# Optimization experiments

Measured on AMD Instinct MI355X. Metric: run time of the kernel, lower is better.

The kernel has to match this reference:

```python
import jax, jax.numpy as jnp
import numpy as np

B, LQ, C = 4, 4096, 384
NH, NL, NP = 6, 1, 4
HL, WL = 64, 64
LV = HL * WL
DH = C // NH
EPS = 1e-6


def layer_norm(x, g, b):
    mu = jnp.mean(x, axis=-1, keepdims=True)
    var = jnp.mean(jnp.square(x - mu), axis=-1, keepdims=True)
    return (x - mu) * jax.lax.rsqrt(var + EPS) * g + b


def ms_deform_attn_core(value, spatial_shapes, level_start_index, loc, attn_w):
    # value [B,LV,NH,DH]; loc [B,LQ,NH,NL,NP,2] in [0,1]; attn_w [B,LQ,NH,NL,NP]
    ss = np.asarray(spatial_shapes)
    lsi = np.asarray(level_start_index)
    Bv, _, nH, dh = value.shape
    Lq = loc.shape[1]
    nP = loc.shape[4]
    out = jnp.zeros((Bv, Lq, nH, dh), value.dtype)
    for l in range(loc.shape[3]):
        Hl, Wl = int(ss[l, 0]), int(ss[l, 1])
        st = int(lsi[l])
        vflat = value[:, st:st + Hl * Wl]  # [B, Hl*Wl, nH, dh]
        xy = loc[:, :, :, l]               # [B,LQ,nH,NP,2]
        # grid_sample(align_corners=False): pixel = loc * size - 0.5
        x = xy[..., 0] * Wl - 0.5
        y = xy[..., 1] * Hl - 0.5
        x0 = jnp.floor(x)
        y0 = jnp.floor(y)
        wx = x - x0
        wy = y - y0
        x0i = x0.astype(jnp.int32)
        y0i = y0.astype(jnp.int32)

        def gather(xi, yi):
            # zero padding outside the feature map (padding_mode='zeros')
            valid = (xi >= 0) & (xi < Wl) & (yi >= 0) & (yi < Hl)
            idx = jnp.clip(yi, 0, Hl - 1) * Wl + jnp.clip(xi, 0, Wl - 1)  # [B,LQ,nH,NP]
            idx2 = idx.transpose(0, 1, 3, 2).reshape(Bv, Lq * nP, nH)
            g = jnp.take_along_axis(vflat, idx2[..., None], axis=1)       # [B,LQ*NP,nH,dh]
            g = g.reshape(Bv, Lq, nP, nH, dh).transpose(0, 1, 3, 2, 4)    # [B,LQ,nH,NP,dh]
            return g * valid[..., None].astype(value.dtype)

        samp = (gather(x0i, y0i) * ((1 - wx) * (1 - wy))[..., None]
                + gather(x0i + 1, y0i) * (wx * (1 - wy))[..., None]
                + gather(x0i, y0i + 1) * ((1 - wx) * wy)[..., None]
                + gather(x0i + 1, y0i + 1) * (wx * wy)[..., None])
        out = out + jnp.einsum('bqhpd,bqhp->bqhd', samp, attn_w[:, :, :, l])
    return out.reshape(Bv, Lq, nH * dh)


def setup_inputs() -> dict:
    key = jax.random.key(0)
    ks = jax.random.split(key, 12)
    s = 0.02
    return {
        'query': jax.random.normal(ks[0], (B, LQ, C), jnp.float32),
        'reference_points': jax.random.uniform(ks[1], (B, LQ, NL, 2), dtype=jnp.float32),
        'feat': jax.random.normal(ks[2], (B, LV, C), jnp.float32),
        'spatial_shapes': jnp.array([[HL, WL]], jnp.int32),
        'level_start_index': jnp.array([0], jnp.int32),
        'ln_q_g': jnp.ones((C,), jnp.float32), 'ln_q_b': jnp.zeros((C,), jnp.float32),
        'ln_f_g': jnp.ones((C,), jnp.float32), 'ln_f_b': jnp.zeros((C,), jnp.float32),
        'gamma': jax.random.normal(ks[3], (C,), jnp.float32) * 0.1,
        'Wv': jax.random.normal(ks[4], (C, C), jnp.float32) * s,
        'bv': jnp.zeros((C,), jnp.float32),
        'Wo': jax.random.normal(ks[5], (C, NH * NL * NP * 2), jnp.float32) * s,
        'bo': jax.random.normal(ks[6], (NH * NL * NP * 2,), jnp.float32) * 0.5,
        'Wa': jax.random.normal(ks[7], (C, NH * NL * NP), jnp.float32) * s,
        'ba': jnp.zeros((NH * NL * NP,), jnp.float32),
        'Wout': jax.random.normal(ks[8], (C, C), jnp.float32) * s,
        'bout': jnp.zeros((C,), jnp.float32),
    }


def reference(query, reference_points, feat, spatial_shapes, level_start_index,
              ln_q_g, ln_q_b, ln_f_g, ln_f_b, gamma,
              Wv, bv, Wo, bo, Wa, ba, Wout, bout):
    q = layer_norm(query, ln_q_g, ln_q_b)
    f = layer_norm(feat, ln_f_g, ln_f_b)
    value = (f @ Wv + bv).reshape(B, LV, NH, DH)
    offsets = (q @ Wo + bo).reshape(B, LQ, NH, NL, NP, 2)
    attn_w = jax.nn.softmax((q @ Wa + ba).reshape(B, LQ, NH, NL * NP), axis=-1)
    attn_w = attn_w.reshape(B, LQ, NH, NL, NP)
    # offset normalizer is (W, H) per level
    norm = jnp.stack([spatial_shapes[:, 1], spatial_shapes[:, 0]], -1).astype(jnp.float32)
    loc = reference_points[:, :, None, :, None, :] + offsets / norm[None, None, None, :, None, :]
    attn = ms_deform_attn_core(value, spatial_shapes, level_start_index, loc, attn_w)
    attn = attn @ Wout + bout
    return query + gamma * attn
```

## Files before the change

### kernel.cpp

```cpp
#include <hip/hip_runtime.h>
#include <math.h>

#define B_    4
#define LQ_   4096
#define C_    384
#define NH_   6
#define NP_   4
#define HL_   64
#define WL_   64
#define LV_   (HL_ * WL_)
#define ROWS_ (B_ * LQ_)
#define EPS_  1e-6f
#define NOFF_ 48
#define NLOG_ 24
#define WCTR_ 96

typedef unsigned short u16;
typedef unsigned int   u32;
typedef __bf16 bf16x8 __attribute__((ext_vector_type(8)));
typedef float  f32x4  __attribute__((ext_vector_type(4)));

__device__ __forceinline__ u16 f2bf(float f) {
    u32 u = __float_as_uint(f);
    u += 0x7fff + ((u >> 16) & 1);
    return (u16)(u >> 16);
}
__device__ __forceinline__ u32 pack2bf(float a, float b) {
    return (u32)f2bf(a) | ((u32)f2bf(b) << 16);
}

__device__ __forceinline__ f32x4 mfma16(bf16x8 a, bf16x8 b, f32x4 c) {
    return __builtin_amdgcn_mfma_f32_16x16x32_bf16(a, b, c, 0, 0, 0);
}

__device__ __forceinline__ void gl_lds16(const u16* g, u16* l) {
    __builtin_amdgcn_global_load_lds(
        (const __attribute__((address_space(1))) unsigned int*)g,
        (__attribute__((address_space(3))) unsigned int*)l, 16, 0, 0);
}

__device__ __forceinline__ void vm_wait8() { asm volatile("s_waitcnt vmcnt(8)" ::: "memory"); }
__device__ __forceinline__ void vm_wait7() { asm volatile("s_waitcnt vmcnt(7)" ::: "memory"); }
__device__ __forceinline__ void vm_wait0() { asm volatile("s_waitcnt vmcnt(0)" ::: "memory"); }
__device__ __forceinline__ void lgkm0()    { asm volatile("s_waitcnt lgkmcnt(0)" ::: "memory"); }
__device__ __forceinline__ void barrier_() { asm volatile("s_barrier" ::: "memory"); }

#define LN_BLOCKS_   8192
#define PREP_BLOCKS_ 1297

__global__ __launch_bounds__(256) void ln_prep(
    const float* __restrict__ query, const float* __restrict__ feat,
    const float* __restrict__ qg, const float* __restrict__ qbv,
    const float* __restrict__ fg, const float* __restrict__ fbv,
    u16* __restrict__ qout, u16* __restrict__ fout,
    const float* __restrict__ Wv, const float* __restrict__ Wout,
    const float* __restrict__ Wo, const float* __restrict__ Wa,
    const float* __restrict__ bo, const float* __restrict__ ba,
    u16* __restrict__ WvT, u16* __restrict__ WoutT, u16* __restrict__ WcT,
    float* __restrict__ bias_c)
{
    if (blockIdx.x < LN_BLOCKS_) {
        int wid  = threadIdx.x >> 6;
        int lane = threadIdx.x & 63;
        int row  = blockIdx.x * 4 + wid;
        const float *src, *g, *bsh;
        u16* dst;
        int r;
        if (row < ROWS_) { src = query; g = qg; bsh = qbv; dst = qout; r = row; }
        else             { src = feat;  g = fg; bsh = fbv; dst = fout; r = row - ROWS_; }

        const float* x = src + (size_t)r * C_;
        float4 a4 = *(const float4*)(x + 4 * lane);
        float2 a2 = *(const float2*)(x + 256 + 2 * lane);
        float v0 = a4.x, v1 = a4.y, v2 = a4.z, v3 = a4.w, v4 = a2.x, v5 = a2.y;

        float s = v0 + v1 + v2 + v3 + v4 + v5;
#pragma unroll
        for (int off = 32; off; off >>= 1) s += __shfl_xor(s, off);
        float mu = s * (1.f / C_);

        float d0 = v0 - mu, d1 = v1 - mu, d2 = v2 - mu;
        float d3 = v3 - mu, d4 = v4 - mu, d5 = v5 - mu;
        float s2 = d0*d0 + d1*d1 + d2*d2 + d3*d3 + d4*d4 + d5*d5;
#pragma unroll
        for (int off = 32; off; off >>= 1) s2 += __shfl_xor(s2, off);
        float rs = rsqrtf(s2 * (1.f / C_) + EPS_);

        float4 g4 = *(const float4*)(g + 4 * lane);
        float4 b4 = *(const float4*)(bsh + 4 * lane);
        float2 g2 = *(const float2*)(g + 256 + 2 * lane);
        float2 b2 = *(const float2*)(bsh + 256 + 2 * lane);

        float o0 = d0 * rs * g4.x + b4.x;
        float o1 = d1 * rs * g4.y + b4.y;
        float o2 = d2 * rs * g4.z + b4.z;
        float o3 = d3 * rs * g4.w + b4.w;
        float o4 = d4 * rs * g2.x + b2.x;
        float o5 = d5 * rs * g2.y + b2.y;

        u16* y = dst + (size_t)r * C_;
        uint2 w0; w0.x = pack2bf(o0, o1); w0.y = pack2bf(o2, o3);
        *(uint2*)(y + 4 * lane) = w0;
        *(u32*)(y + 256 + 2 * lane) = pack2bf(o4, o5);
    } else {
        const int KN = 384 * 384;
        int idx = (blockIdx.x - LN_BLOCKS_) * 256 + threadIdx.x;
        if (idx < KN) {
            int n = idx / 384, k = idx - n * 384;
            WvT[idx] = f2bf(Wv[k * 384 + n]);
        } else if (idx < 2 * KN) {
            int t = idx - KN;
            int n = t / 384, k = t - n * 384;
            WoutT[t] = f2bf(Wout[k * 384 + n]);
        } else if (idx < 2 * KN + WCTR_ * 384) {
            int t = idx - 2 * KN;
            int n = t / 384, k = t - n * 384;
            float v = (n < 48) ? Wo[k * 48 + n] : (n < 72 ? Wa[k * 24 + (n - 48)] : 0.f);
            WcT[t] = f2bf(v);
        } else if (idx < 2 * KN + WCTR_ * 384 + 80) {
            int n = idx - (2 * KN + WCTR_ * 384);
            bias_c[n] = (n < 48) ? bo[n] : (n < 72 ? ba[n - 48] : 0.f);
        }
    }
}

__global__ __launch_bounds__(256) void gemm_combined(
    const u16* __restrict__ fb, const u16* __restrict__ qb,
    const u16* __restrict__ WvT, const u16* __restrict__ WcT,
    const float* __restrict__ bv, const float* __restrict__ bias_c,
    u16* __restrict__ valb, float* __restrict__ offs, float* __restrict__ logits)
{
    __shared__ __align__(16) u16 As_[2][8192];
    __shared__ __align__(16) u16 Bs_[2][8192];

    int g    = blockIdx.x;
    int tid  = threadIdx.x;
    int lane = tid & 63, wid = tid >> 6;
    int fr = lane & 15, quad = lane >> 4;

    int swz  = (fr & 7) * 8;
    int off0 = (quad * 8) ^ swz;

    int srow = tid >> 3;
    int csw  = ((tid & 7) ^ (srow & 7)) * 8;

    if (g < 384) {
        int m0 = (g & 127) * 128, n0 = (g >> 7) * 128;
        const u16* aSrc = fb  + (size_t)(m0 + srow) * 384 + csw;
        const u16* bSrc = WvT + (size_t)(n0 + srow) * 384 + csw;

        int wm = (wid >> 1) * 64, wn = (wid & 1) * 64;

        f32x4 zero = {0.f, 0.f, 0.f, 0.f};
        f32x4 acc[4][4];
#pragma unroll
        for (int i = 0; i < 4; ++i)
#pragma unroll
            for (int j = 0; j < 4; ++j) acc[i][j] = zero;

#define STGV(bu, t) { _Pragma("unroll") for (int l = 0; l < 4; ++l) { \
            gl_lds16(aSrc + (size_t)l * (32*384) + (t)*64, &As_[bu][tid*8 + l*2048]); \
            gl_lds16(bSrc + (size_t)l * (32*384) + (t)*64, &Bs_[bu][tid*8 + l*2048]); } }

        STGV(0, 0)
        STGV(1, 1)
#pragma unroll
        for (int t = 0; t < 6; ++t) {
            const int bu = t & 1;
            if (t < 5) vm_wait8(); else vm_wait0();
            barrier_();
            bf16x8 af[4][2], bfr[4][2];
#pragma unroll
            for (int i = 0; i < 4; ++i) {
                int ra = (wm + i * 16 + fr) * 64;
                af[i][0]  = *(const bf16x8*)&As_[bu][ra + off0];
                af[i][1]  = *(const bf16x8*)&As_[bu][ra + (off0 ^ 32)];
                int rb = (wn + i * 16 + fr) * 64;
                bfr[i][0] = *(const bf16x8*)&Bs_[bu][rb + off0];
                bfr[i][1] = *(const bf16x8*)&Bs_[bu][rb + (off0 ^ 32)];
            }
            lgkm0();
            barrier_();
            if (t < 4) STGV(bu, t + 2)
#pragma unroll
            for (int i = 0; i < 4; ++i)
#pragma unroll
                for (int j = 0; j < 4; ++j) {
                    acc[i][j] = mfma16(af[i][0], bfr[j][0], acc[i][j]);
                    acc[i][j] = mfma16(af[i][1], bfr[j][1], acc[i][j]);
                }
        }
#undef STGV

#pragma unroll
        for (int i = 0; i < 4; ++i) {
            int row = m0 + wm + i * 16 + quad * 4;
#pragma unroll
            for (int j = 0; j < 4; ++j) {
                int col = n0 + wn + j * 16 + fr;
                float bcol = bv[col];
#pragma unroll
                for (int r = 0; r < 4; ++r)
                    valb[(size_t)(row + r) * C_ + col] = f2bf(acc[i][j][r] + bcol);
            }
        }
    } else {
        int m0 = (g - 384) * 128;
        const u16* aSrc = qb  + (size_t)(m0 + srow) * 384 + csw;
        const u16* bSrc = WcT + (size_t)srow * 384 + csw;

        int wm = wid * 32;

        f32x4 zero = {0.f, 0.f, 0.f, 0.f};
        f32x4 acc[2][5];
#pragma unroll
        for (int i = 0; i < 2; ++i)
#pragma unroll
            for (int j = 0; j < 5; ++j) acc[i][j] = zero;

#define STGS(bu, t) { _Pragma("unroll") for (int l = 0; l < 4; ++l) \
            gl_lds16(aSrc + (size_t)l * (32*384) + (t)*64, &As_[bu][tid*8 + l*2048]); \
            _Pragma("unroll") for (int l = 0; l < 3; ++l) \
            gl_lds16(bSrc + (size_t)l * (32*384) + (t)*64, &Bs_[bu][tid*8 + l*2048]); }

        STGS(0, 0)
        STGS(1, 1)
#pragma unroll
        for (int t = 0; t < 6; ++t) {
            const int bu = t & 1;
            if (t < 5) vm_wait7(); else vm_wait0();
            barrier_();
            bf16x8 af[2][2], bfr[5][2];
#pragma unroll
            for (int i = 0; i < 2; ++i) {
                int ra = (wm + i * 16 + fr) * 64;
                af[i][0] = *(const bf16x8*)&As_[bu][ra + off0];
                af[i][1] = *(const bf16x8*)&As_[bu][ra + (off0 ^ 32)];
            }
#pragma unroll
            for (int j = 0; j < 5; ++j) {
                int rb = (j * 16 + fr) * 64;
                bfr[j][0] = *(const bf16x8*)&Bs_[bu][rb + off0];
                bfr[j][1] = *(const bf16x8*)&Bs_[bu][rb + (off0 ^ 32)];
            }
            lgkm0();
            barrier_();
            if (t < 4) STGS(bu, t + 2)
#pragma unroll
            for (int i = 0; i < 2; ++i)
#pragma unroll
                for (int j = 0; j < 5; ++j) {
                    acc[i][j] = mfma16(af[i][0], bfr[j][0], acc[i][j]);
                    acc[i][j] = mfma16(af[i][1], bfr[j][1], acc[i][j]);
                }
        }
#undef STGS

#pragma unroll
        for (int i = 0; i < 2; ++i) {
            int row = m0 + wm + i * 16 + quad * 4;
#pragma unroll
            for (int j = 0; j < 5; ++j) {
                int col = j * 16 + fr;
                if (col < 72) {
                    float bcol = bias_c[col];
#pragma unroll
                    for (int r = 0; r < 4; ++r) {
                        float v = acc[i][j][r] + bcol;
                        if (col < 48) offs[(size_t)(row + r) * NOFF_ + col] = v;
                        else          logits[(size_t)(row + r) * NLOG_ + (col - 48)] = v;
                    }
                }
            }
        }
    }
}

__global__ __launch_bounds__(384) void sampler(
    const u16*  __restrict__ value,
    const float* __restrict__ rp,
    const float* __restrict__ offs,
    const float* __restrict__ logits,
    u16* __restrict__ attn)
{
    int t = threadIdx.x;
    int g = blockIdx.x;
    int b     = (g & 7) >> 1;
    int local = ((g >> 3) << 1) | (g & 1);
    int q  = t / 48, dc = t - q * 48;
    int h  = dc >> 3;
    int col0 = dc << 3;
    int r  = b * LQ_ + local * 8 + q;

    float4 lg  = *(const float4*)(logits + (size_t)r * NLOG_ + h * 4);
    float2 rpv = *(const float2*)(rp + (size_t)r * 2);
    float4 of0 = *(const float4*)(offs + (size_t)r * NOFF_ + h * 8);
    float4 of1 = *(const float4*)(offs + (size_t)r * NOFF_ + h * 8 + 4);

    float mx = fmaxf(fmaxf(lg.x, lg.y), fmaxf(lg.z, lg.w));
    float e0 = __expf(lg.x - mx), e1 = __expf(lg.y - mx);
    float e2 = __expf(lg.z - mx), e3 = __expf(lg.w - mx);
    float rden = 1.f / (e0 + e1 + e2 + e3);
    float aws[4] = {e0 * rden, e1 * rden, e2 * rden, e3 * rden};
    float oxs[4] = {of0.x, of0.z, of1.x, of1.z};
    float oys[4] = {of0.y, of0.w, of1.y, of1.w};

    const u16* vbase = value + (size_t)b * LV_ * C_ + col0;
    float acc[8] = {0.f, 0.f, 0.f, 0.f, 0.f, 0.f, 0.f, 0.f};
#pragma unroll
    for (int p = 0; p < NP_; ++p) {
        float x = rpv.x * (float)WL_ + oxs[p] - 0.5f;
        float y = rpv.y * (float)HL_ + oys[p] - 0.5f;
        float x0f = floorf(x), y0f = floorf(y);
        float wx = x - x0f, wy = y - y0f;
        int x0 = (int)x0f, y0 = (int)y0f;
#pragma unroll
        for (int c = 0; c < 4; ++c) {
            int xi = x0 + (c & 1);
            int yi = y0 + (c >> 1);
            bool valid = (xi >= 0) && (xi < WL_) && (yi >= 0) && (yi < HL_);
            int xc = xi < 0 ? 0 : (xi > WL_ - 1 ? WL_ - 1 : xi);
            int yc = yi < 0 ? 0 : (yi > HL_ - 1 ? HL_ - 1 : yi);
            float w = ((c & 1) ? wx : 1.f - wx) * ((c >> 1) ? wy : 1.f - wy) * aws[p];
            w = valid ? w : 0.f;
            bf16x8 vv = *(const bf16x8*)(vbase + (size_t)(yc * WL_ + xc) * C_);
#pragma unroll
            for (int e = 0; e < 8; ++e) acc[e] += w * (float)vv[e];
        }
    }

    uint4 o;
    o.x = pack2bf(acc[0], acc[1]);
    o.y = pack2bf(acc[2], acc[3]);
    o.z = pack2bf(acc[4], acc[5]);
    o.w = pack2bf(acc[6], acc[7]);
    *(uint4*)(attn + (size_t)r * C_ + col0) = o;
}

__global__ __launch_bounds__(256) void out_gemm(
    const u16* __restrict__ A, const u16* __restrict__ Bt,
    const float* __restrict__ bout, const float* __restrict__ gamma,
    const float* __restrict__ query, float* __restrict__ out)
{
    __shared__ __align__(16) u16 As_[2][8192];
    __shared__ __align__(16) u16 Bs_[2][8192];

    int g    = blockIdx.x;
    int tid  = threadIdx.x;
    int lane = tid & 63, wid = tid >> 6;
    int fr = lane & 15, quad = lane >> 4;

    int swz  = (fr & 7) * 8;
    int off0 = (quad * 8) ^ swz;
    int srow = tid >> 3;
    int csw  = ((tid & 7) ^ (srow & 7)) * 8;

    int m0 = (g & 127) * 128, n0 = (g >> 7) * 96;
    const u16* aSrc = A  + (size_t)(m0 + srow) * 384 + csw;
    const u16* bSrc = Bt + (size_t)(n0 + srow) * 384 + csw;

    int wm = (wid >> 1) * 64, wn = (wid & 1) * 48;

    f32x4 zero = {0.f, 0.f, 0.f, 0.f};
    f32x4 acc[4][3];
#pragma unroll
    for (int i = 0; i < 4; ++i)
#pragma unroll
        for (int j = 0; j < 3; ++j) acc[i][j] = zero;

#define STGO(bu, t) { _Pragma("unroll") for (int l = 0; l < 4; ++l) \
        gl_lds16(aSrc + (size_t)l * (32*384) + (t)*64, &As_[bu][tid*8 + l*2048]); \
        _Pragma("unroll") for (int l = 0; l < 3; ++l) \
        gl_lds16(bSrc + (size_t)l * (32*384) + (t)*64, &Bs_[bu][tid*8 + l*2048]); }

    STGO(0, 0)
    STGO(1, 1)
#pragma unroll
    for (int t = 0; t < 6; ++t) {
        const int bu = t & 1;
        if (t < 5) vm_wait7(); else vm_wait0();
        barrier_();
        bf16x8 af[4][2], bfr[3][2];
#pragma unroll
        for (int i = 0; i < 4; ++i) {
            int ra = (wm + i * 16 + fr) * 64;
            af[i][0] = *(const bf16x8*)&As_[bu][ra + off0];
            af[i][1] = *(const bf16x8*)&As_[bu][ra + (off0 ^ 32)];
        }
#pragma unroll
        for (int j = 0; j < 3; ++j) {
            int rb = (wn + j * 16 + fr) * 64;
            bfr[j][0] = *(const bf16x8*)&Bs_[bu][rb + off0];
            bfr[j][1] = *(const bf16x8*)&Bs_[bu][rb + (off0 ^ 32)];
        }
        lgkm0();
        barrier_();
        if (t < 4) STGO(bu, t + 2)
#pragma unroll
        for (int i = 0; i < 4; ++i)
#pragma unroll
            for (int j = 0; j < 3; ++j) {
                acc[i][j] = mfma16(af[i][0], bfr[j][0], acc[i][j]);
                acc[i][j] = mfma16(af[i][1], bfr[j][1], acc[i][j]);
            }
    }
#undef STGO

#pragma unroll
    for (int i = 0; i < 4; ++i) {
        int row = m0 + wm + i * 16 + quad * 4;
#pragma unroll
        for (int j = 0; j < 3; ++j) {
            int col = n0 + wn + j * 16 + fr;
            float bc = bout[col], gm = gamma[col];
#pragma unroll
            for (int r = 0; r < 4; ++r) {
                size_t o = (size_t)(row + r) * C_ + col;
                out[o] = query[o] + gm * (acc[i][j][r] + bc);
            }
        }
    }
}

extern "C" void kernel_launch(void* const* d_in, const int* in_sizes, int n_in,
                              void* d_out, int out_size, void* d_ws, size_t ws_size,
                              hipStream_t stream)
{
    const float* query  = (const float*)d_in[0];
    const float* rp     = (const float*)d_in[1];
    const float* feat   = (const float*)d_in[2];
    const float* gamma  = (const float*)d_in[9];
    const float* Wv     = (const float*)d_in[10];
    const float* bv     = (const float*)d_in[11];
    const float* Wo     = (const float*)d_in[12];
    const float* bo     = (const float*)d_in[13];
    const float* Wa     = (const float*)d_in[14];
    const float* ba     = (const float*)d_in[15];
    const float* Wout   = (const float*)d_in[16];
    const float* bout   = (const float*)d_in[17];
    float* out = (float*)d_out;

    u16* wsu    = (u16*)d_ws;
    u16* qb     = wsu;
    u16* fb     = qb    + (size_t)ROWS_ * C_;
    u16* valb   = fb    + (size_t)ROWS_ * C_;
    u16* attnb  = valb  + (size_t)ROWS_ * C_;
    u16* WvT    = attnb + (size_t)ROWS_ * C_;
    u16* WoutT  = WvT   + 384 * 384;
    u16* WcT    = WoutT + 384 * 384;
    float* offs   = (float*)(WcT + WCTR_ * 384);
    float* logits = offs + (size_t)ROWS_ * NOFF_;
    float* bias_c = logits + (size_t)ROWS_ * NLOG_;

    ln_prep<<<LN_BLOCKS_ + PREP_BLOCKS_, 256, 0, stream>>>(
        query, feat,
        (const float*)d_in[5], (const float*)d_in[6],
        (const float*)d_in[7], (const float*)d_in[8],
        qb, fb, Wv, Wout, Wo, Wa, bo, ba, WvT, WoutT, WcT, bias_c);

    gemm_combined<<<512, 256, 0, stream>>>(fb, qb, WvT, WcT, bv, bias_c,
                                           valb, offs, logits);

    sampler<<<2048, 384, 0, stream>>>(valb, rp, offs, logits, attnb);

    out_gemm<<<512, 256, 0, stream>>>(attnb, WoutT, bout, gamma, query, out);
}
```

Measured before the change: 162.2 us.

## Fuse layernorms into the projection GEMM kernel prologue

Moves the query and feature layernorms out of the prep kernel into the start of the combined GEMM kernel. Each wave normalizes 32 rows of its tile's A strip, writes bf16 to global memory, then waits and barriers before loading that strip into LDS. This removes the separate layernorm pass over the whole activation set. In exchange, the feature layernorm is recomputed by all three N-tile blocks that share an M tile. Those blocks also write identical values to the same buffer, and the row loop runs serially per wave ahead of the GEMM.

Result: slower. 189.1 us (+16.5%).

```diff
diff --git a/kernel.cpp b/kernel.cpp
--- a/kernel.cpp
+++ b/kernel.cpp
@@ -45,30 +45,42 @@
 __device__ __forceinline__ void lgkm0()    { asm volatile("s_waitcnt lgkmcnt(0)" ::: "memory"); }
 __device__ __forceinline__ void barrier_() { asm volatile("s_barrier" ::: "memory"); }
 
-#define LN_BLOCKS_   8192
 #define PREP_BLOCKS_ 1297
 
-__global__ __launch_bounds__(256) void ln_prep(
-    const float* __restrict__ query, const float* __restrict__ feat,
-    const float* __restrict__ qg, const float* __restrict__ qbv,
-    const float* __restrict__ fg, const float* __restrict__ fbv,
-    u16* __restrict__ qout, u16* __restrict__ fout,
+__global__ __launch_bounds__(256) void prep(
     const float* __restrict__ Wv, const float* __restrict__ Wout,
     const float* __restrict__ Wo, const float* __restrict__ Wa,
     const float* __restrict__ bo, const float* __restrict__ ba,
     u16* __restrict__ WvT, u16* __restrict__ WoutT, u16* __restrict__ WcT,
     float* __restrict__ bias_c)
 {
-    if (blockIdx.x < LN_BLOCKS_) {
-        int wid  = threadIdx.x >> 6;
-        int lane = threadIdx.x & 63;
-        int row  = blockIdx.x * 4 + wid;
-        const float *src, *g, *bsh;
-        u16* dst;
-        int r;
-        if (row < ROWS_) { src = query; g = qg; bsh = qbv; dst = qout; r = row; }
-        else             { src = feat;  g = fg; bsh = fbv; dst = fout; r = row - ROWS_; }
-
+    const int KN = 384 * 384;
+    int idx = blockIdx.x * 256 + threadIdx.x;
+    if (idx < KN) {
+        int n = idx / 384, k = idx - n * 384;
+        WvT[idx] = f2bf(Wv[k * 384 + n]);
+    } else if (idx < 2 * KN) {
+        int t = idx - KN;
+        int n = t / 384, k = t - n * 384;
+        WoutT[t] = f2bf(Wout[k * 384 + n]);
+    } else if (idx < 2 * KN + WCTR_ * 384) {
+        int t = idx - 2 * KN;
+        int n = t / 384, k = t - n * 384;
+        float v = (n < 48) ? Wo[k * 48 + n] : (n < 72 ? Wa[k * 24 + (n - 48)] : 0.f);
+        WcT[t] = f2bf(v);
+    } else if (idx < 2 * KN + WCTR_ * 384 + 80) {
+        int n = idx - (2 * KN + WCTR_ * 384);
+        bias_c[n] = (n < 48) ? bo[n] : (n < 72 ? ba[n - 48] : 0.f);
+    }
+}
+
+__device__ __forceinline__ void ln_strip32(const float* __restrict__ src,
+                                           u16* __restrict__ dst,
+                                           int base, int lane,
+                                           float4 g4, float4 b4, float2 g2, float2 b2)
+{
+    for (int i = 0; i < 32; ++i) {
+        int r = base + i;
         const float* x = src + (size_t)r * C_;
         float4 a4 = *(const float4*)(x + 4 * lane);
         float2 a2 = *(const float2*)(x + 256 + 2 * lane);
@@ -85,11 +97,6 @@
 #pragma unroll
         for (int off = 32; off; off >>= 1) s2 += __shfl_xor(s2, off);
         float rs = rsqrtf(s2 * (1.f / C_) + EPS_);
-
-        float4 g4 = *(const float4*)(g + 4 * lane);
-        float4 b4 = *(const float4*)(bsh + 4 * lane);
-        float2 g2 = *(const float2*)(g + 256 + 2 * lane);
-        float2 b2 = *(const float2*)(bsh + 256 + 2 * lane);
 
         float o0 = d0 * rs * g4.x + b4.x;
         float o1 = d1 * rs * g4.y + b4.y;
@@ -102,30 +109,14 @@
         uint2 w0; w0.x = pack2bf(o0, o1); w0.y = pack2bf(o2, o3);
         *(uint2*)(y + 4 * lane) = w0;
         *(u32*)(y + 256 + 2 * lane) = pack2bf(o4, o5);
-    } else {
-        const int KN = 384 * 384;
-        int idx = (blockIdx.x - LN_BLOCKS_) * 256 + threadIdx.x;
-        if (idx < KN) {
-            int n = idx / 384, k = idx - n * 384;
-            WvT[idx] = f2bf(Wv[k * 384 + n]);
-        } else if (idx < 2 * KN) {
-            int t = idx - KN;
-            int n = t / 384, k = t - n * 384;
-            WoutT[t] = f2bf(Wout[k * 384 + n]);
-        } else if (idx < 2 * KN + WCTR_ * 384) {
-            int t = idx - 2 * KN;
-            int n = t / 384, k = t - n * 384;
-            float v = (n < 48) ? Wo[k * 48 + n] : (n < 72 ? Wa[k * 24 + (n - 48)] : 0.f);
-            WcT[t] = f2bf(v);
-        } else if (idx < 2 * KN + WCTR_ * 384 + 80) {
-            int n = idx - (2 * KN + WCTR_ * 384);
-            bias_c[n] = (n < 48) ? bo[n] : (n < 72 ? ba[n - 48] : 0.f);
-        }
     }
 }
 
 __global__ __launch_bounds__(256) void gemm_combined(
-    const u16* __restrict__ fb, const u16* __restrict__ qb,
+    const float* __restrict__ query, const float* __restrict__ feat,
+    const float* __restrict__ qg, const float* __restrict__ qbv,
+    const float* __restrict__ fg, const float* __restrict__ fbv,
+    u16* __restrict__ qb, u16* __restrict__ fb,
     const u16* __restrict__ WvT, const u16* __restrict__ WcT,
     const float* __restrict__ bv, const float* __restrict__ bias_c,
     u16* __restrict__ valb, float* __restrict__ offs, float* __restrict__ logits)
@@ -140,12 +131,22 @@
 
     int swz  = (fr & 7) * 8;
     int off0 = (quad * 8) ^ swz;
-
     int srow = tid >> 3;
     int csw  = ((tid & 7) ^ (srow & 7)) * 8;
 
     if (g < 384) {
         int m0 = (g & 127) * 128, n0 = (g >> 7) * 128;
+
+        {
+            float4 g4 = *(const float4*)(fg + 4 * lane);
+            float4 b4 = *(const float4*)(fbv + 4 * lane);
+            float2 g2 = *(const float2*)(fg + 256 + 2 * lane);
+            float2 b2 = *(const float2*)(fbv + 256 + 2 * lane);
+            ln_strip32(feat, fb, m0 + wid * 32, lane, g4, b4, g2, b2);
+        }
+        vm_wait0();
+        barrier_();
+
         const u16* aSrc = fb  + (size_t)(m0 + srow) * 384 + csw;
         const u16* bSrc = WvT + (size_t)(n0 + srow) * 384 + csw;
 
@@ -206,6 +207,17 @@
         }
     } else {
         int m0 = (g - 384) * 128;
+
+        {
+            float4 g4 = *(const float4*)(qg + 4 * lane);
+            float4 b4 = *(const float4*)(qbv + 4 * lane);
+            float2 g2 = *(const float2*)(qg + 256 + 2 * lane);
+            float2 b2 = *(const float2*)(qbv + 256 + 2 * lane);
+            ln_strip32(query, qb, m0 + wid * 32, lane, g4, b4, g2, b2);
+        }
+        vm_wait0();
+        barrier_();
+
         const u16* aSrc = qb  + (size_t)(m0 + srow) * 384 + csw;
         const u16* bSrc = WcT + (size_t)srow * 384 + csw;
 
@@ -429,6 +441,10 @@
     const float* query  = (const float*)d_in[0];
     const float* rp     = (const float*)d_in[1];
     const float* feat   = (const float*)d_in[2];
+    const float* qg     = (const float*)d_in[5];
+    const float* qbv    = (const float*)d_in[6];
+    const float* fg     = (const float*)d_in[7];
+    const float* fbv    = (const float*)d_in[8];
     const float* gamma  = (const float*)d_in[9];
     const float* Wv     = (const float*)d_in[10];
     const float* bv     = (const float*)d_in[11];
@@ -452,13 +468,11 @@
     float* logits = offs + (size_t)ROWS_ * NOFF_;
     float* bias_c = logits + (size_t)ROWS_ * NLOG_;
 
-    ln_prep<<<LN_BLOCKS_ + PREP_BLOCKS_, 256, 0, stream>>>(
-        query, feat,
-        (const float*)d_in[5], (const float*)d_in[6],
-        (const float*)d_in[7], (const float*)d_in[8],
-        qb, fb, Wv, Wout, Wo, Wa, bo, ba, WvT, WoutT, WcT, bias_c);
-
-    gemm_combined<<<512, 256, 0, stream>>>(fb, qb, WvT, WcT, bv, bias_c,
+    prep<<<PREP_BLOCKS_, 256, 0, stream>>>(Wv, Wout, Wo, Wa, bo, ba,
+                                           WvT, WoutT, WcT, bias_c);
+
+    gemm_combined<<<512, 256, 0, stream>>>(query, feat, qg, qbv, fg, fbv,
+                                           qb, fb, WvT, WcT, bv, bias_c,
                                            valb, offs, logits);
 
     sampler<<<2048, 384, 0, stream>>>(valb, rp, offs, logits, attnb);
```

## Halve GEMM K-tile to 32 with unswizzled LDS and 12-stage pipeline

Applied to the files above, without the earlier changes.

All three MFMA GEMMs now stage K in chunks of 32 instead of 64, halving the LDS buffers and doubling the number of pipeline iterations. Each thread issues four 16-byte global-to-LDS loads per stage, and the XOR swizzle on LDS addresses is dropped in favour of a plain 32-element row stride. The combined weight is padded to 128 rows so the staging pattern stays uniform. The smaller shared footprint is meant to raise occupancy, at the cost of more barriers per tile and possible LDS bank conflicts from the unswizzled layout.

Result: slower. 176.9 us (+9.1%).

```diff
diff --git a/kernel.cpp b/kernel.cpp
--- a/kernel.cpp
+++ b/kernel.cpp
@@ -13,7 +13,7 @@
 #define EPS_  1e-6f
 #define NOFF_ 48
 #define NLOG_ 24
-#define WCTR_ 96
+#define WCTR_ 128
 
 typedef unsigned short u16;
 typedef unsigned int   u32;
@@ -39,14 +39,13 @@
         (__attribute__((address_space(3))) unsigned int*)l, 16, 0, 0);
 }
 
-__device__ __forceinline__ void vm_wait8() { asm volatile("s_waitcnt vmcnt(8)" ::: "memory"); }
-__device__ __forceinline__ void vm_wait7() { asm volatile("s_waitcnt vmcnt(7)" ::: "memory"); }
+__device__ __forceinline__ void vm_wait4() { asm volatile("s_waitcnt vmcnt(4)" ::: "memory"); }
 __device__ __forceinline__ void vm_wait0() { asm volatile("s_waitcnt vmcnt(0)" ::: "memory"); }
 __device__ __forceinline__ void lgkm0()    { asm volatile("s_waitcnt lgkmcnt(0)" ::: "memory"); }
 __device__ __forceinline__ void barrier_() { asm volatile("s_barrier" ::: "memory"); }
 
 #define LN_BLOCKS_   8192
-#define PREP_BLOCKS_ 1297
+#define PREP_BLOCKS_ 1345
 
 __global__ __launch_bounds__(256) void ln_prep(
     const float* __restrict__ query, const float* __restrict__ feat,
@@ -130,24 +129,21 @@
     const float* __restrict__ bv, const float* __restrict__ bias_c,
     u16* __restrict__ valb, float* __restrict__ offs, float* __restrict__ logits)
 {
-    __shared__ __align__(16) u16 As_[2][8192];
-    __shared__ __align__(16) u16 Bs_[2][8192];
+    __shared__ __align__(16) u16 As_[2][4096];
+    __shared__ __align__(16) u16 Bs_[2][4096];
 
     int g    = blockIdx.x;
     int tid  = threadIdx.x;
     int lane = tid & 63, wid = tid >> 6;
     int fr = lane & 15, quad = lane >> 4;
 
-    int swz  = (fr & 7) * 8;
-    int off0 = (quad * 8) ^ swz;
-
-    int srow = tid >> 3;
-    int csw  = ((tid & 7) ^ (srow & 7)) * 8;
+    int srow = tid >> 2;
+    int scol = (tid & 3) * 8;
 
     if (g < 384) {
         int m0 = (g & 127) * 128, n0 = (g >> 7) * 128;
-        const u16* aSrc = fb  + (size_t)(m0 + srow) * 384 + csw;
-        const u16* bSrc = WvT + (size_t)(n0 + srow) * 384 + csw;
+        const u16* aSrc = fb  + (size_t)(m0 + srow) * 384 + scol;
+        const u16* bSrc = WvT + (size_t)(n0 + srow) * 384 + scol;
 
         int wm = (wid >> 1) * 64, wn = (wid & 1) * 64;
 
@@ -158,37 +154,33 @@
 #pragma unroll
             for (int j = 0; j < 4; ++j) acc[i][j] = zero;
 
-#define STGV(bu, t) { _Pragma("unroll") for (int l = 0; l < 4; ++l) { \
-            gl_lds16(aSrc + (size_t)l * (32*384) + (t)*64, &As_[bu][tid*8 + l*2048]); \
-            gl_lds16(bSrc + (size_t)l * (32*384) + (t)*64, &Bs_[bu][tid*8 + l*2048]); } }
+#define STGV(bu, t) { \
+            gl_lds16(aSrc + (t)*32,            &As_[bu][tid*8]); \
+            gl_lds16(aSrc + 64*384 + (t)*32,   &As_[bu][tid*8 + 2048]); \
+            gl_lds16(bSrc + (t)*32,            &Bs_[bu][tid*8]); \
+            gl_lds16(bSrc + 64*384 + (t)*32,   &Bs_[bu][tid*8 + 2048]); }
 
         STGV(0, 0)
         STGV(1, 1)
 #pragma unroll
-        for (int t = 0; t < 6; ++t) {
+        for (int t = 0; t < 12; ++t) {
             const int bu = t & 1;
-            if (t < 5) vm_wait8(); else vm_wait0();
+            if (t < 11) vm_wait4(); else vm_wait0();
             barrier_();
-            bf16x8 af[4][2], bfr[4][2];
+            bf16x8 af[4], bfr[4];
 #pragma unroll
             for (int i = 0; i < 4; ++i) {
-                int ra = (wm + i * 16 + fr) * 64;
-                af[i][0]  = *(const bf16x8*)&As_[bu][ra + off0];
-                af[i][1]  = *(const bf16x8*)&As_[bu][ra + (off0 ^ 32)];
-                int rb = (wn + i * 16 + fr) * 64;
-                bfr[i][0] = *(const bf16x8*)&Bs_[bu][rb + off0];
-                bfr[i][1] = *(const bf16x8*)&Bs_[bu][rb + (off0 ^ 32)];
+                af[i]  = *(const bf16x8*)&As_[bu][(wm + i * 16 + fr) * 32 + quad * 8];
+                bfr[i] = *(const bf16x8*)&Bs_[bu][(wn + i * 16 + fr) * 32 + quad * 8];
             }
             lgkm0();
             barrier_();
-            if (t < 4) STGV(bu, t + 2)
+            if (t < 10) STGV(bu, t + 2)
 #pragma unroll
             for (int i = 0; i < 4; ++i)
 #pragma unroll
-                for (int j = 0; j < 4; ++j) {
-                    acc[i][j] = mfma16(af[i][0], bfr[j][0], acc[i][j]);
-                    acc[i][j] = mfma16(af[i][1], bfr[j][1], acc[i][j]);
-                }
+                for (int j = 0; j < 4; ++j)
+                    acc[i][j] = mfma16(af[i], bfr[j], acc[i][j]);
         }
 #undef STGV
 
@@ -206,8 +198,8 @@
         }
     } else {
         int m0 = (g - 384) * 128;
-        const u16* aSrc = qb  + (size_t)(m0 + srow) * 384 + csw;
-        const u16* bSrc = WcT + (size_t)srow * 384 + csw;
+        const u16* aSrc = qb  + (size_t)(m0 + srow) * 384 + scol;
+        const u16* bSrc = WcT + (size_t)srow * 384 + scol;
 
         int wm = wid * 32;
 
@@ -218,41 +210,34 @@
 #pragma unroll
             for (int j = 0; j < 5; ++j) acc[i][j] = zero;
 
-#define STGS(bu, t) { _Pragma("unroll") for (int l = 0; l < 4; ++l) \
-            gl_lds16(aSrc + (size_t)l * (32*384) + (t)*64, &As_[bu][tid*8 + l*2048]); \
-            _Pragma("unroll") for (int l = 0; l < 3; ++l) \
-            gl_lds16(bSrc + (size_t)l * (32*384) + (t)*64, &Bs_[bu][tid*8 + l*2048]); }
+#define STGS(bu, t) { \
+            gl_lds16(aSrc + (t)*32,            &As_[bu][tid*8]); \
+            gl_lds16(aSrc + 64*384 + (t)*32,   &As_[bu][tid*8 + 2048]); \
+            gl_lds16(bSrc + (t)*32,            &Bs_[bu][tid*8]); \
+            gl_lds16(bSrc + 64*384 + (t)*32,   &Bs_[bu][tid*8 + 2048]); }
 
         STGS(0, 0)
         STGS(1, 1)
 #pragma unroll
-        for (int t = 0; t < 6; ++t) {
+        for (int t = 0; t < 12; ++t) {
             const int bu = t & 1;
-            if (t < 5) vm_wait7(); else vm_wait0();
+            if (t < 11) vm_wait4(); else vm_wait0();
             barrier_();
-            bf16x8 af[2][2], bfr[5][2];
-#pragma unroll
-            for (int i = 0; i < 2; ++i) {
-                int ra = (wm + i * 16 + fr) * 64;
-                af[i][0] = *(const bf16x8*)&As_[bu][ra + off0];
-                af[i][1] = *(const bf16x8*)&As_[bu][ra + (off0 ^ 32)];
-            }
-#pragma unroll
-            for (int j = 0; j < 5; ++j) {
-                int rb = (j * 16 + fr) * 64;
-                bfr[j][0] = *(const bf16x8*)&Bs_[bu][rb + off0];
-                bfr[j][1] = *(const bf16x8*)&Bs_[bu][rb + (off0 ^ 32)];
-            }
+            bf16x8 af[2], bfr[5];
+#pragma unroll
+            for (int i = 0; i < 2; ++i)
+                af[i] = *(const bf16x8*)&As_[bu][(wm + i * 16 + fr) * 32 + quad * 8];
+#pragma unroll
+            for (int j = 0; j < 5; ++j)
+                bfr[j] = *(const bf16x8*)&Bs_[bu][(j * 16 + fr) * 32 + quad * 8];
             lgkm0();
             barrier_();
-            if (t < 4) STGS(bu, t + 2)
+            if (t < 10) STGS(bu, t + 2)
 #pragma unroll
             for (int i = 0; i < 2; ++i)
 #pragma unroll
-                for (int j = 0; j < 5; ++j) {
-                    acc[i][j] = mfma16(af[i][0], bfr[j][0], acc[i][j]);
-                    acc[i][j] = mfma16(af[i][1], bfr[j][1], acc[i][j]);
-                }
+                for (int j = 0; j < 5; ++j)
+                    acc[i][j] = mfma16(af[i], bfr[j], acc[i][j]);
         }
 #undef STGS
 
@@ -342,22 +327,20 @@
     const float* __restrict__ bout, const float* __restrict__ gamma,
     const float* __restrict__ query, float* __restrict__ out)
 {
-    __shared__ __align__(16) u16 As_[2][8192];
-    __shared__ __align__(16) u16 Bs_[2][8192];
+    __shared__ __align__(16) u16 As_[2][4096];
+    __shared__ __align__(16) u16 Bs_[2][4096];
 
     int g    = blockIdx.x;
     int tid  = threadIdx.x;
     int lane = tid & 63, wid = tid >> 6;
     int fr = lane & 15, quad = lane >> 4;
 
-    int swz  = (fr & 7) * 8;
-    int off0 = (quad * 8) ^ swz;
-    int srow = tid >> 3;
-    int csw  = ((tid & 7) ^ (srow & 7)) * 8;
+    int srow = tid >> 2;
+    int scol = (tid & 3) * 8;
 
     int m0 = (g & 127) * 128, n0 = (g >> 7) * 96;
-    const u16* aSrc = A  + (size_t)(m0 + srow) * 384 + csw;
-    const u16* bSrc = Bt + (size_t)(n0 + srow) * 384 + csw;
+    const u16* aSrc = A  + (size_t)(m0 + srow) * 384 + scol;
+    const u16* bSrc = Bt + (size_t)(n0 + srow) * 384 + scol;
 
     int wm = (wid >> 1) * 64, wn = (wid & 1) * 48;
 
@@ -368,41 +351,34 @@
 #pragma unroll
         for (int j = 0; j < 3; ++j) acc[i][j] = zero;
 
-#define STGO(bu, t) { _Pragma("unroll") for (int l = 0; l < 4; ++l) \
-        gl_lds16(aSrc + (size_t)l * (32*384) + (t)*64, &As_[bu][tid*8 + l*2048]); \
-        _Pragma("unroll") for (int l = 0; l < 3; ++l) \
-        gl_lds16(bSrc + (size_t)l * (32*384) + (t)*64, &Bs_[bu][tid*8 + l*2048]); }
+#define STGO(bu, t) { \
+        gl_lds16(aSrc + (t)*32,            &As_[bu][tid*8]); \
+        gl_lds16(aSrc + 64*384 + (t)*32,   &As_[bu][tid*8 + 2048]); \
+        gl_lds16(bSrc + (t)*32,            &Bs_[bu][tid*8]); \
+        gl_lds16(bSrc + 64*384 + (t)*32,   &Bs_[bu][tid*8 + 2048]); }
 
     STGO(0, 0)
     STGO(1, 1)
 #pragma unroll
-    for (int t = 0; t < 6; ++t) {
+    for (int t = 0; t < 12; ++t) {
         const int bu = t & 1;
-        if (t < 5) vm_wait7(); else vm_wait0();
+        if (t < 11) vm_wait4(); else vm_wait0();
         barrier_();
-        bf16x8 af[4][2], bfr[3][2];
-#pragma unroll
-        for (int i = 0; i < 4; ++i) {
-            int ra = (wm + i * 16 + fr) * 64;
-            af[i][0] = *(const bf16x8*)&As_[bu][ra + off0];
-            af[i][1] = *(const bf16x8*)&As_[bu][ra + (off0 ^ 32)];
-        }
-#pragma unroll
-        for (int j = 0; j < 3; ++j) {
-            int rb = (wn + j * 16 + fr) * 64;
-            bfr[j][0] = *(const bf16x8*)&Bs_[bu][rb + off0];
-            bfr[j][1] = *(const bf16x8*)&Bs_[bu][rb + (off0 ^ 32)];
-        }
+        bf16x8 af[4], bfr[3];
+#pragma unroll
+        for (int i = 0; i < 4; ++i)
+            af[i] = *(const bf16x8*)&As_[bu][(wm + i * 16 + fr) * 32 + quad * 8];
+#pragma unroll
+        for (int j = 0; j < 3; ++j)
+            bfr[j] = *(const bf16x8*)&Bs_[bu][(wn + j * 16 + fr) * 32 + quad * 8];
         lgkm0();
         barrier_();
-        if (t < 4) STGO(bu, t + 2)
+        if (t < 10) STGO(bu, t + 2)
 #pragma unroll
         for (int i = 0; i < 4; ++i)
 #pragma unroll
-            for (int j = 0; j < 3; ++j) {
-                acc[i][j] = mfma16(af[i][0], bfr[j][0], acc[i][j]);
-                acc[i][j] = mfma16(af[i][1], bfr[j][1], acc[i][j]);
-            }
+            for (int j = 0; j < 3; ++j)
+                acc[i][j] = mfma16(af[i], bfr[j], acc[i][j]);
     }
 #undef STGO
 
@@ -447,7 +423,7 @@
     u16* attnb  = valb  + (size_t)ROWS_ * C_;
     u16* WvT    = attnb + (size_t)ROWS_ * C_;
     u16* WoutT  = WvT   + 384 * 384;
-    u16* WcT    = WoutT + 384 * 384;
+    u16* WcT    = WoutT + 512 * 384;
     float* offs   = (float*)(WcT + WCTR_ * 384);
     float* logits = offs + (size_t)ROWS_ * NOFF_;
     float* bias_c = logits + (size_t)ROWS_ * NLOG_;
```

## Fuse deformable sampler into output projection GEMM via LDS-resident attention tile

Applied to the files above, without the earlier changes.

Merges the sampler and output GEMM into one kernel: each 512-thread block samples 64 query rows into a swizzled LDS tile, then multiplies it by Wout streamed through double-buffered LDS. This removes the bf16 attention round-trip through global memory and one launch. In exchange the grid shrinks to 256 blocks with large LDS use, which lowers occupancy and latency hiding for the gather-heavy sampling phase, and each block now reloads the full Wout.

After: 163.9 us. No clear change (+1.0%).

```diff
diff --git a/kernel.cpp b/kernel.cpp
--- a/kernel.cpp
+++ b/kernel.cpp
@@ -41,6 +41,7 @@
 
 __device__ __forceinline__ void vm_wait8() { asm volatile("s_waitcnt vmcnt(8)" ::: "memory"); }
 __device__ __forceinline__ void vm_wait7() { asm volatile("s_waitcnt vmcnt(7)" ::: "memory"); }
+__device__ __forceinline__ void vm_wait6() { asm volatile("s_waitcnt vmcnt(6)" ::: "memory"); }
 __device__ __forceinline__ void vm_wait0() { asm volatile("s_waitcnt vmcnt(0)" ::: "memory"); }
 __device__ __forceinline__ void lgkm0()    { asm volatile("s_waitcnt lgkmcnt(0)" ::: "memory"); }
 __device__ __forceinline__ void barrier_() { asm volatile("s_barrier" ::: "memory"); }
@@ -140,7 +141,6 @@
 
     int swz  = (fr & 7) * 8;
     int off0 = (quad * 8) ^ swz;
-
     int srow = tid >> 3;
     int csw  = ((tid & 7) ^ (srow & 7)) * 8;
 
@@ -276,91 +276,96 @@
     }
 }
 
-__global__ __launch_bounds__(384) void sampler(
-    const u16*  __restrict__ value,
+__global__ __launch_bounds__(512) void sample_out(
+    const u16*  __restrict__ valb,
     const float* __restrict__ rp,
     const float* __restrict__ offs,
     const float* __restrict__ logits,
-    u16* __restrict__ attn)
-{
-    int t = threadIdx.x;
-    int g = blockIdx.x;
-    int b     = (g & 7) >> 1;
-    int local = ((g >> 3) << 1) | (g & 1);
-    int q  = t / 48, dc = t - q * 48;
-    int h  = dc >> 3;
-    int col0 = dc << 3;
-    int r  = b * LQ_ + local * 8 + q;
-
-    float4 lg  = *(const float4*)(logits + (size_t)r * NLOG_ + h * 4);
-    float2 rpv = *(const float2*)(rp + (size_t)r * 2);
-    float4 of0 = *(const float4*)(offs + (size_t)r * NOFF_ + h * 8);
-    float4 of1 = *(const float4*)(offs + (size_t)r * NOFF_ + h * 8 + 4);
-
-    float mx = fmaxf(fmaxf(lg.x, lg.y), fmaxf(lg.z, lg.w));
-    float e0 = __expf(lg.x - mx), e1 = __expf(lg.y - mx);
-    float e2 = __expf(lg.z - mx), e3 = __expf(lg.w - mx);
-    float rden = 1.f / (e0 + e1 + e2 + e3);
-    float aws[4] = {e0 * rden, e1 * rden, e2 * rden, e3 * rden};
-    float oxs[4] = {of0.x, of0.z, of1.x, of1.z};
-    float oys[4] = {of0.y, of0.w, of1.y, of1.w};
-
-    const u16* vbase = value + (size_t)b * LV_ * C_ + col0;
-    float acc[8] = {0.f, 0.f, 0.f, 0.f, 0.f, 0.f, 0.f, 0.f};
-#pragma unroll
-    for (int p = 0; p < NP_; ++p) {
-        float x = rpv.x * (float)WL_ + oxs[p] - 0.5f;
-        float y = rpv.y * (float)HL_ + oys[p] - 0.5f;
-        float x0f = floorf(x), y0f = floorf(y);
-        float wx = x - x0f, wy = y - y0f;
-        int x0 = (int)x0f, y0 = (int)y0f;
-#pragma unroll
-        for (int c = 0; c < 4; ++c) {
-            int xi = x0 + (c & 1);
-            int yi = y0 + (c >> 1);
-            bool valid = (xi >= 0) && (xi < WL_) && (yi >= 0) && (yi < HL_);
-            int xc = xi < 0 ? 0 : (xi > WL_ - 1 ? WL_ - 1 : xi);
-            int yc = yi < 0 ? 0 : (yi > HL_ - 1 ? HL_ - 1 : yi);
-            float w = ((c & 1) ? wx : 1.f - wx) * ((c >> 1) ? wy : 1.f - wy) * aws[p];
-            w = valid ? w : 0.f;
-            bf16x8 vv = *(const bf16x8*)(vbase + (size_t)(yc * WL_ + xc) * C_);
-#pragma unroll
-            for (int e = 0; e < 8; ++e) acc[e] += w * (float)vv[e];
-        }
-    }
-
-    uint4 o;
-    o.x = pack2bf(acc[0], acc[1]);
-    o.y = pack2bf(acc[2], acc[3]);
-    o.z = pack2bf(acc[4], acc[5]);
-    o.w = pack2bf(acc[6], acc[7]);
-    *(uint4*)(attn + (size_t)r * C_ + col0) = o;
-}
-
-__global__ __launch_bounds__(256) void out_gemm(
-    const u16* __restrict__ A, const u16* __restrict__ Bt,
+    const u16* __restrict__ WoutT,
     const float* __restrict__ bout, const float* __restrict__ gamma,
     const float* __restrict__ query, float* __restrict__ out)
 {
-    __shared__ __align__(16) u16 As_[2][8192];
-    __shared__ __align__(16) u16 Bs_[2][8192];
+    __shared__ __align__(16) u16 Al[64 * 384];
+    __shared__ __align__(16) u16 Bs_[2][384 * 64];
 
     int g    = blockIdx.x;
     int tid  = threadIdx.x;
     int lane = tid & 63, wid = tid >> 6;
     int fr = lane & 15, quad = lane >> 4;
 
-    int swz  = (fr & 7) * 8;
-    int off0 = (quad * 8) ^ swz;
+    int b     = (g & 7) >> 1;
+    int local = ((g >> 3) << 1) | (g & 1);
+    int row0  = b * LQ_ + local * 64;
+
     int srow = tid >> 3;
     int csw  = ((tid & 7) ^ (srow & 7)) * 8;
-
-    int m0 = (g & 127) * 128, n0 = (g >> 7) * 96;
-    const u16* aSrc = A  + (size_t)(m0 + srow) * 384 + csw;
-    const u16* bSrc = Bt + (size_t)(n0 + srow) * 384 + csw;
-
-    int wm = (wid >> 1) * 64, wn = (wid & 1) * 48;
-
+    const u16* bSrc = WoutT + (size_t)srow * 384 + csw;
+
+#define STGB(bu, t) { _Pragma("unroll") for (int l = 0; l < 6; ++l) \
+    gl_lds16(bSrc + (size_t)l * (64*384) + (t)*64, &Bs_[bu][tid*8 + l*4096]); }
+
+    STGB(0, 0)
+    STGB(1, 1)
+
+    const u16* vbat = valb + (size_t)b * LV_ * C_;
+#pragma unroll
+    for (int it = 0; it < 6; ++it) {
+        int c   = tid + 512 * it;
+        int row = c / 48, dc = c - row * 48;
+        int h   = dc >> 3;
+        int col0 = dc << 3;
+        int r   = row0 + row;
+
+        float4 lg  = *(const float4*)(logits + (size_t)r * NLOG_ + h * 4);
+        float2 rpv = *(const float2*)(rp + (size_t)r * 2);
+        float4 of0 = *(const float4*)(offs + (size_t)r * NOFF_ + h * 8);
+        float4 of1 = *(const float4*)(offs + (size_t)r * NOFF_ + h * 8 + 4);
+
+        float mx = fmaxf(fmaxf(lg.x, lg.y), fmaxf(lg.z, lg.w));
+        float e0 = __expf(lg.x - mx), e1 = __expf(lg.y - mx);
+        float e2 = __expf(lg.z - mx), e3 = __expf(lg.w - mx);
+        float rden = 1.f / (e0 + e1 + e2 + e3);
+        float aws[4] = {e0 * rden, e1 * rden, e2 * rden, e3 * rden};
+        float oxs[4] = {of0.x, of0.z, of1.x, of1.z};
+        float oys[4] = {of0.y, of0.w, of1.y, of1.y};
+        oys[3] = of1.w;
+        oys[0] = of0.y; oys[1] = of0.w; oys[2] = of1.y;
+
+        const u16* vbase = vbat + col0;
+        float acc8[8] = {0.f, 0.f, 0.f, 0.f, 0.f, 0.f, 0.f, 0.f};
+#pragma unroll
+        for (int p = 0; p < NP_; ++p) {
+            float x = rpv.x * (float)WL_ + oxs[p] - 0.5f;
+            float y = rpv.y * (float)HL_ + oys[p] - 0.5f;
+            float x0f = floorf(x), y0f = floorf(y);
+            float wx = x - x0f, wy = y - y0f;
+            int x0 = (int)x0f, y0 = (int)y0f;
+#pragma unroll
+            for (int cc = 0; cc < 4; ++cc) {
+                int xi = x0 + (cc & 1);
+                int yi = y0 + (cc >> 1);
+                bool valid = (xi >= 0) && (xi < WL_) && (yi >= 0) && (yi < HL_);
+                int xc = xi < 0 ? 0 : (xi > WL_ - 1 ? WL_ - 1 : xi);
+                int yc = yi < 0 ? 0 : (yi > HL_ - 1 ? HL_ - 1 : yi);
+                float w = ((cc & 1) ? wx : 1.f - wx) * ((cc >> 1) ? wy : 1.f - wy) * aws[p];
+                w = valid ? w : 0.f;
+                bf16x8 vv = *(const bf16x8*)(vbase + (size_t)(yc * WL_ + xc) * C_);
+#pragma unroll
+                for (int e = 0; e < 8; ++e) acc8[e] += w * (float)vv[e];
+            }
+        }
+
+        uint4 o;
+        o.x = pack2bf(acc8[0], acc8[1]);
+        o.y = pack2bf(acc8[2], acc8[3]);
+        o.z = pack2bf(acc8[4], acc8[5]);
+        o.w = pack2bf(acc8[6], acc8[7]);
+        *(uint4*)&Al[row * 384 + ((dc ^ (row & 7)) << 3)] = o;
+    }
+    lgkm0();
+
+    int wn = wid * 48;
+    int fs = fr & 7;
     f32x4 zero = {0.f, 0.f, 0.f, 0.f};
     f32x4 acc[4][3];
 #pragma unroll
@@ -368,24 +373,19 @@
 #pragma unroll
         for (int j = 0; j < 3; ++j) acc[i][j] = zero;
 
-#define STGO(bu, t) { _Pragma("unroll") for (int l = 0; l < 4; ++l) \
-        gl_lds16(aSrc + (size_t)l * (32*384) + (t)*64, &As_[bu][tid*8 + l*2048]); \
-        _Pragma("unroll") for (int l = 0; l < 3; ++l) \
-        gl_lds16(bSrc + (size_t)l * (32*384) + (t)*64, &Bs_[bu][tid*8 + l*2048]); }
-
-    STGO(0, 0)
-    STGO(1, 1)
+    int off0 = (quad * 8) ^ (fs * 8);
+
 #pragma unroll
     for (int t = 0; t < 6; ++t) {
         const int bu = t & 1;
-        if (t < 5) vm_wait7(); else vm_wait0();
+        if (t < 5) vm_wait6(); else vm_wait0();
         barrier_();
         bf16x8 af[4][2], bfr[3][2];
 #pragma unroll
         for (int i = 0; i < 4; ++i) {
-            int ra = (wm + i * 16 + fr) * 64;
-            af[i][0] = *(const bf16x8*)&As_[bu][ra + off0];
-            af[i][1] = *(const bf16x8*)&As_[bu][ra + (off0 ^ 32)];
+            int ra = (i * 16 + fr) * 384;
+            af[i][0] = *(const bf16x8*)&Al[ra + (((t * 8 + quad) ^ fs) << 3)];
+            af[i][1] = *(const bf16x8*)&Al[ra + (((t * 8 + 4 + quad) ^ fs) << 3)];
         }
 #pragma unroll
         for (int j = 0; j < 3; ++j) {
@@ -395,7 +395,7 @@
         }
         lgkm0();
         barrier_();
-        if (t < 4) STGO(bu, t + 2)
+        if (t < 4) STGB(bu, t + 2)
 #pragma unroll
         for (int i = 0; i < 4; ++i)
 #pragma unroll
@@ -404,18 +404,18 @@
                 acc[i][j] = mfma16(af[i][1], bfr[j][1], acc[i][j]);
             }
     }
-#undef STGO
+#undef STGB
 
 #pragma unroll
     for (int i = 0; i < 4; ++i) {
-        int row = m0 + wm + i * 16 + quad * 4;
+        int rowg = row0 + i * 16 + quad * 4;
 #pragma unroll
         for (int j = 0; j < 3; ++j) {
-            int col = n0 + wn + j * 16 + fr;
+            int col = wn + j * 16 + fr;
             float bc = bout[col], gm = gamma[col];
 #pragma unroll
             for (int r = 0; r < 4; ++r) {
-                size_t o = (size_t)(row + r) * C_ + col;
+                size_t o = (size_t)(rowg + r) * C_ + col;
                 out[o] = query[o] + gm * (acc[i][j][r] + bc);
             }
         }
@@ -461,7 +461,6 @@
     gemm_combined<<<512, 256, 0, stream>>>(fb, qb, WvT, WcT, bv, bias_c,
                                            valb, offs, logits);
 
-    sampler<<<2048, 384, 0, stream>>>(valb, rp, offs, logits, attnb);
-
-    out_gemm<<<512, 256, 0, stream>>>(attnb, WoutT, bout, gamma, query, out);
-}
+    sample_out<<<256, 512, 0, stream>>>(valb, rp, offs, logits,
+                                        WoutT, bout, gamma, query, out);
+}
```
